# Kernel optimization log

Measured on AMD Instinct MI355X. Metric: run time of the kernel, lower is better.

The kernel has to match this reference:

```python
import jax, jax.numpy as jnp
import numpy as np

# ---- Cayley-Dickson octonion multiplication tables (SIGN_TABLE, WEIGHT_IDX) ----
def _cd_conj(a):
    n = a.shape[0]
    if n == 1:
        return a
    h = n // 2
    return np.concatenate([_cd_conj(a[:h]), -a[h:]])

def _cd_mul(a, b):
    n = a.shape[0]
    if n == 1:
        return a * b
    h = n // 2
    a1, a2 = a[:h], a[h:]
    c1, c2 = b[:h], b[h:]
    # (a1,a2)(c1,c2) = (a1 c1 - conj(c2) a2, c2 a1 + a2 conj(c1))
    return np.concatenate([_cd_mul(a1, c1) - _cd_mul(_cd_conj(c2), a2),
                           _cd_mul(c2, a1) + _cd_mul(a2, _cd_conj(c1))])

def _octonion_tables():
    signs = np.zeros((8, 8), dtype=np.float32)
    widx = np.zeros((8, 8), dtype=np.int32)
    for i in range(8):
        for j in range(8):
            ei = np.zeros(8); ei[i] = 1.0
            ej = np.zeros(8); ej[j] = 1.0
            p = _cd_mul(ei, ej)
            k = int(np.argmax(np.abs(p)))  # == i ^ j
            signs[i, j] = np.sign(p[k])
            widx[i, j] = k
    return jnp.asarray(signs), jnp.asarray(widx)

SIGNS, WIDX = _octonion_tables()


def ternary_ste(W):
    # BitNet-style per-matrix ternary quantization with straight-through estimator.
    s = jnp.mean(jnp.abs(W), axis=(-2, -1), keepdims=True) + 1e-8
    Wq = jnp.clip(jnp.round(W / s), -1.0, 1.0) * s
    return W + jax.lax.stop_gradient(Wq - W)


def oct_linear(x, W):
    # x: [B,T,C] split into 8 parts of C/8; out_i = sum_j sign[i,j] * x_j @ Wq[i^j]
    B, T, C = x.shape
    c8 = C // 8
    x8 = x.reshape(B, T, 8, c8)
    Wq = ternary_ste(W)          # [8, c8, c8]
    Wg = Wq[WIDX]                # [8, 8, c8, c8]
    out = jnp.einsum('ij,btjc,ijcd->btid', SIGNS, x8, Wg)
    return out.reshape(B, T, C)


def apply_rope(q, freqs_cos, freqs_sin):
    # q: [B,T,H,D]; complex pairs are (q[...,2k], q[...,2k+1])
    qe, qo = q[..., 0::2], q[..., 1::2]
    cos = freqs_cos[None, :, None, :]
    sin = freqs_sin[None, :, None, :]
    oe = qe * cos - qo * sin
    oo = qe * sin + qo * cos
    return jnp.stack([oe, oo], axis=-1).reshape(q.shape)


def setup_inputs() -> dict:
    key = jax.random.key(0)
    ks = jax.random.split(key, 8)
    B, T, C, H = 4, 1024, 2048, 16
    D = C // H           # 128
    c8 = C // 8          # 256
    x = jax.random.normal(ks[0], (B, T, C), dtype=jnp.float32)
    # RoPE tables (theta = 10000)
    inv = 1.0 / (10000.0 ** (jnp.arange(0, D, 2, dtype=jnp.float32) / D))
    ang = jnp.arange(T, dtype=jnp.float32)[:, None] * inv[None, :]   # [T, D/2]
    freqs_cos = jnp.cos(ang)
    freqs_sin = jnp.sin(ang)
    wq = jax.random.normal(ks[1], (8, c8, c8), dtype=jnp.float32) * 0.02
    wk = jax.random.normal(ks[2], (8, c8, c8), dtype=jnp.float32) * 0.02
    wv = jax.random.normal(ks[3], (8, c8, c8), dtype=jnp.float32) * 0.02
    wo = jax.random.normal(ks[4], (8, c8, c8), dtype=jnp.float32) * 0.02
    mixer_W = jax.random.normal(ks[5], (8, D, D), dtype=jnp.float32) * 0.02
    mixer_beta = jnp.ones((D,), dtype=jnp.float32) * 0.1
    return {"x": x, "freqs_cos": freqs_cos, "freqs_sin": freqs_sin,
            "wq": wq, "wk": wk, "wv": wv, "wo": wo,
            "mixer_W": mixer_W, "mixer_beta": mixer_beta}


def reference(x, freqs_cos, freqs_sin, wq, wk, wv, wo, mixer_W, mixer_beta):
    B, T, C = x.shape
    H = 16
    D = C // H
    q = oct_linear(x, wq).reshape(B, T, H, D)
    k = oct_linear(x, wk).reshape(B, T, H, D)
    v = oct_linear(x, wv).reshape(B, T, H, D)
    q = apply_rope(q, freqs_cos, freqs_sin)
    k = apply_rope(k, freqs_cos, freqs_sin)
    q, k, v = (jnp.transpose(t, (0, 2, 1, 3)) for t in (q, k, v))  # [B,H,T,D]
    # causal SDPA
    scale = 1.0 / jnp.sqrt(jnp.asarray(D, dtype=q.dtype))
    scores = jnp.einsum('bhqd,bhkd->bhqk', q, k) * scale
    mask = jnp.tril(jnp.ones((T, T), dtype=bool))
    scores = jnp.where(mask, scores, jnp.asarray(-1e30, dtype=scores.dtype))
    probs = jax.nn.softmax(scores, axis=-1)
    y = jnp.einsum('bhqk,bhkd->bhqd', probs, v)  # [B,H,T,D]
    # octonion head mixing per group of 8 heads
    G = H // 8
    y8 = y.reshape(B, G, 8, T, D)
    Wg = mixer_W[WIDX]  # [8,8,D,D]
    y8 = jnp.einsum('ij,bgjtd,ijde->bgite', SIGNS, y8, Wg) * mixer_beta
    y = y8.reshape(B, H, T, D)
    y = jnp.transpose(y, (0, 2, 1, 3)).reshape(B, T, C)
    return oct_linear(y, wo)
```

## Files before the change

kernel.cpp:

```cpp
#include <hip/hip_runtime.h>
#include <math.h>

#define CDIM 2048
#define QKVW 6144

typedef __bf16 bf16x8 __attribute__((ext_vector_type(8)));
typedef __bf16 bf16x4 __attribute__((ext_vector_type(4)));
typedef float  f32x4  __attribute__((ext_vector_type(4)));
typedef float  f32x16 __attribute__((ext_vector_type(16)));

__device__ __constant__ float SIGNS_c[64] = {
  1,  1,  1,  1,  1,  1,  1,  1,
  1, -1,  1, -1,  1, -1, -1,  1,
  1, -1, -1,  1,  1,  1, -1, -1,
  1,  1, -1, -1,  1, -1,  1, -1,
  1, -1, -1, -1, -1,  1,  1,  1,
  1,  1, -1,  1, -1, -1, -1,  1,
  1,  1,  1, -1, -1,  1, -1, -1,
  1, -1,  1,  1, -1, -1,  1, -1
};

__device__ __forceinline__ void load_lds16(const void* g, void* lp) {
  __builtin_amdgcn_global_load_lds(
      (const __attribute__((address_space(1))) unsigned int*)g,
      (__attribute__((address_space(3))) unsigned int*)lp, 16, 0, 0);
}

__device__ __forceinline__ void wg_barrier() {
  asm volatile("" ::: "memory");
  __builtin_amdgcn_s_barrier();
  asm volatile("" ::: "memory");
}

__device__ __forceinline__ unsigned pack2(float a, float b) {
  union { __bf16 h[2]; unsigned u; } x;
  x.h[0] = (__bf16)a; x.h[1] = (__bf16)b; return x.u;
}

__global__ __launch_bounds__(256)
void cast_scale(const float* __restrict__ x, __bf16* __restrict__ xb,
                const float* __restrict__ wq, const float* __restrict__ wk,
                const float* __restrict__ wv, const float* __restrict__ wo,
                double* __restrict__ part) {
  __shared__ double red[256];
  if (blockIdx.x < 8192) {
    int i = blockIdx.x * 256 + threadIdx.x;
    float4 v = *(const float4*)(x + (size_t)i * 4);
    bf16x4 o;
    o[0] = (__bf16)v.x; o[1] = (__bf16)v.y; o[2] = (__bf16)v.z; o[3] = (__bf16)v.w;
    *(bf16x4*)(xb + (size_t)i * 4) = o;
    return;
  }
  int bid = blockIdx.x - 8192;
  int which = bid >> 6, m = (bid >> 3) & 7, seg = bid & 7;
  const float* W = (which == 0) ? wq : (which == 1) ? wk : (which == 2) ? wv : wo;
  const float4* w4 = (const float4*)(W + (m << 16) + seg * 8192);
  double acc = 0.0;
  #pragma unroll
  for (int i = 0; i < 8; ++i) {
    float4 v = w4[threadIdx.x + i * 256];
    acc += (double)fabsf(v.x) + (double)fabsf(v.y) +
           (double)fabsf(v.z) + (double)fabsf(v.w);
  }
  red[threadIdx.x] = acc;
  __syncthreads();
  for (int s = 128; s > 0; s >>= 1) {
    if (threadIdx.x < s) red[threadIdx.x] += red[threadIdx.x + s];
    __syncthreads();
  }
  if (threadIdx.x == 0) part[bid] = red[0];
}

__global__ void scale_fin(const double* __restrict__ part, double* __restrict__ s8,
                          double* __restrict__ rs8) {
  int t = threadIdx.x;
  if (t < 32) {
    double a = 0.0;
    #pragma unroll
    for (int i = 0; i < 8; ++i) a += part[t * 8 + i];
    double s = a / 65536.0 + 1e-8;
    s8[t] = s;
    rs8[t] = 1.0 / s;
  }
}

__global__ void build_oct3(const float* __restrict__ wq, const float* __restrict__ wk,
                           const float* __restrict__ wv, const double* __restrict__ s8,
                           const double* __restrict__ rs8, __bf16* __restrict__ MT) {
  int z = blockIdx.y;
  const float* W = (z == 0) ? wq : (z == 1) ? wk : wv;
  const double* sp = s8 + z * 8;
  const double* rp = rs8 + z * 8;
  __bf16* out = MT + (size_t)z * 4194304;
  int idx = blockIdx.x * 256 + threadIdx.x;
  int row = idx & 2047, col = idx >> 11;
  int i = col >> 8, d = col & 255, j = row >> 8, c = row & 255;
  int m = i ^ j;
  double q = rint((double)W[(m << 16) + (c << 8) + d] * rp[m]);
  q = fmin(fmax(q, -1.0), 1.0);
  out[idx] = (__bf16)(SIGNS_c[i * 8 + j] * (float)(q * sp[m]));
}

__global__ void build_wo_mix(const float* __restrict__ W, const double* __restrict__ s8,
                             const double* __restrict__ rs8, __bf16* __restrict__ MT,
                             const float* __restrict__ Wm, const float* __restrict__ beta,
                             __bf16* __restrict__ Mmix) {
  if (blockIdx.x < 16384) {
    int idx = blockIdx.x * 256 + threadIdx.x;
    int row = idx & 2047, col = idx >> 11;
    int i = col >> 8, d = col & 255, j = row >> 8, c = row & 255;
    int m = i ^ j;
    double q = rint((double)W[(m << 16) + (c << 8) + d] * rs8[m]);
    q = fmin(fmax(q, -1.0), 1.0);
    MT[idx] = (__bf16)(SIGNS_c[i * 8 + j] * (float)(q * s8[m]));
    return;
  }
  int idx = (blockIdx.x - 16384) * 256 + threadIdx.x;
  int kl = idx & 1023, kpl = idx >> 10;
  int j = kpl >> 7, dd = kpl & 127;
  int i = kl >> 7, e = kl & 127;
  Mmix[idx] = (__bf16)(SIGNS_c[i * 8 + j] * Wm[((i ^ j) << 14) + (dd << 7) + e] * beta[e]);
}

__global__ __launch_bounds__(512, 2)
void gemm_qkv8(const __bf16* __restrict__ A, const __bf16* __restrict__ BT,
               __bf16* __restrict__ C, __bf16* __restrict__ VT) {
  __shared__ __align__(16) char smem[131072];
  int tid = threadIdx.x;
  int w = tid >> 6, l = tid & 63, hi = l >> 4, lo = l & 15;
  int wm = w >> 2, wn = w & 3;
  int lin = blockIdx.x;
  int xcd = lin & 7, idx = lin >> 3;
  int cy = xcd >> 2, cx = xcd & 3;
  int iby = idx >> 3, ibx = idx & 7;
  int bm = (cy * 8 + iby) * 256;
  int bn = (cx * 8 + ibx) * 192;
  const char* Ab = (const char*)A + (size_t)bm * 4096;
  const char* Bb = (const char*)BT + (size_t)bn * 4096;

  int sw = (((lo & 1) << 2) + hi) ^ (lo >> 1);

  int se_r[2], se_g[2], se_rb[2];
  #pragma unroll
  for (int q = 0; q < 2; ++q) {
    int e = q * 512 + tid;
    int lr = e >> 3, sl = e & 7;
    int x = sl ^ (lr & 7);
    se_r[q] = lr * 2 + (x >> 2);
    se_g[q] = x & 3;
    se_rb[q] = se_r[q] < 192 ? se_r[q] : 191;
  }
  int dstoff[2] = { (0 * 512 + w * 64) * 16, (1 * 512 + w * 64) * 16 };

  f32x4 acc[8][3];
  #pragma unroll
  for (int m = 0; m < 8; ++m)
    #pragma unroll
    for (int n = 0; n < 3; ++n) acc[m][n] = (f32x4){0.f, 0.f, 0.f, 0.f};
  bf16x8 bfr[3];

  #define STG(MAT, TT, KH) do {                                                  \
    char* dst_ = smem + ((TT) & 1) * 65536 + (MAT) * 32768 + (KH) * 16384;       \
    const char* gb_ = (MAT) ? Bb : Ab;                                           \
    _Pragma("unroll")                                                            \
    for (int q = 0; q < 2; ++q) {                                                \
      int r_ = (MAT) ? se_rb[q] : se_r[q];                                       \
      load_lds16(gb_ + (size_t)r_ * 4096 + ((TT) * 64 + (KH) * 32) * 2 + se_g[q] * 16, \
                 dst_ + dstoff[q]);                                              \
    }                                                                            \
  } while (0)

  #define QUAD(TT, KH, MSUB, READB) do {                                         \
    const char* ar_ = smem + ((TT) & 1) * 65536 + (KH) * 16384;                  \
    const char* br_ = ar_ + 32768;                                               \
    if (READB) {                                                                 \
      _Pragma("unroll")                                                          \
      for (int n = 0; n < 3; ++n)                                                \
        bfr[n] = *(const bf16x8*)(br_ + (wn * 24 + n * 8 + (lo >> 1)) * 128 + sw * 16); \
    }                                                                            \
    bf16x8 afr[4];                                                               \
    _Pragma("unroll")                                                            \
    for (int m = 0; m < 4; ++m)                                                  \
      afr[m] = *(const bf16x8*)(ar_ + (wm * 64 + (MSUB) * 32 + m * 8 + (lo >> 1)) * 128 + sw * 16); \
    __builtin_amdgcn_s_setprio(1);                                               \
    _Pragma("unroll")                                                            \
    for (int m = 0; m < 4; ++m)                                                  \
      _Pragma("unroll")                                                          \
      for (int n = 0; n < 3; ++n)                                                \
        acc[(MSUB) * 4 + m][n] =                                                 \
            __builtin_amdgcn_mfma_f32_16x16x32_bf16(afr[m], bfr[n], acc[(MSUB) * 4 + m][n], 0, 0, 0); \
    __builtin_amdgcn_s_setprio(0);                                               \
  } while (0)

  #define LGK0() asm volatile("s_waitcnt lgkmcnt(0)" ::: "memory")
  #define VMW8() asm volatile("s_waitcnt vmcnt(8)" ::: "memory")
  #define VMW4() asm volatile("s_waitcnt vmcnt(4)" ::: "memory")
  #define VMW0() asm volatile("s_waitcnt vmcnt(0)" ::: "memory")

  STG(0, 0, 0); STG(1, 0, 0);
  STG(0, 0, 1); STG(1, 0, 1);
  STG(0, 1, 0); STG(1, 1, 0);
  VMW8();
  wg_barrier();

  #define GITER(T0, LAST) do {                                                   \
     STG(0, (T0) + 1, 1); QUAD((T0), 0, 0, 1); wg_barrier();            \
     STG(1, (T0) + 1, 1); QUAD((T0), 0, 1, 0); LGK0(); VMW8(); wg_barrier(); \
     if (!(LAST)) { STG(0, (T0) + 2, 0); } QUAD((T0), 1, 0, 1); wg_barrier(); \
     if (!(LAST)) { STG(1, (T0) + 2, 0); } QUAD((T0), 1, 1, 0); LGK0(); \
              if (LAST) { VMW4(); } else { VMW8(); } wg_barrier();               \
     if (!(LAST)) { STG(0, (T0) + 2, 1); } QUAD((T0) + 1, 0, 0, 1); wg_barrier(); \
     if (!(LAST)) { STG(1, (T0) + 2, 1); } QUAD((T0) + 1, 0, 1, 0); LGK0(); \
              if (LAST) { VMW0(); } else { VMW8(); } wg_barrier();               \
     if (!(LAST)) { STG(0, (T0) + 3, 0); } QUAD((T0) + 1, 1, 0, 1); wg_barrier(); \
     if (!(LAST)) { STG(1, (T0) + 3, 0); } QUAD((T0) + 1, 1, 1, 0);     \
              if (!(LAST)) { LGK0(); VMW8(); wg_barrier(); }                     \
  } while (0)

  for (int i = 0; i < 15; ++i) GITER(2 * i, false);
  GITER(30, true);

  #undef GITER
  #undef STG
  #undef QUAD
  #undef VMW8
  #undef VMW4
  #undef LGK0
  #undef VMW0

  #pragma unroll
  for (int mm = 0; mm < 8; ++mm)
    #pragma unroll
    for (int n = 0; n < 3; ++n) {
      int col = bn + wn * 48 + n * 16 + lo;
      int row0 = bm + wm * 128 + mm * 16 + hi * 4;
      if (col < 4096) {
        #pragma unroll
        for (int r = 0; r < 4; ++r)
          C[(size_t)(row0 + r) * QKVW + col] = (__bf16)acc[mm][n][r];
      } else {
        int v = col - 4096;
        int bh = (row0 >> 10) * 16 + (v >> 7);
        int dd = v & 127;
        int t0 = row0 & 1023;
        bf16x4 ov;
        #pragma unroll
        for (int r = 0; r < 4; ++r) ov[r] = (__bf16)acc[mm][n][r];
        *(bf16x4*)(VT + ((size_t)bh * 128 + dd) * 1024 + t0) = ov;
      }
    }
}

__global__ __launch_bounds__(512, 2)
void gemm_fin8(const __bf16* __restrict__ A, const __bf16* __restrict__ BT,
               float* __restrict__ C) {
  __shared__ __align__(16) char smem[98304];
  int tid = threadIdx.x;
  int w = tid >> 6, l = tid & 63, hi = l >> 4, lo = l & 15;
  int wm = w >> 2, wn = w & 3;
  int lin = blockIdx.x;
  int xcd = lin & 7, idx = lin >> 3;
  int cy = xcd >> 1, cx = xcd & 1;
  int iby = idx >> 2, ibx = idx & 3;
  int bm = (cy * 8 + iby) * 128;
  int bn = (cx * 4 + ibx) * 256;
  const char* Ab = (const char*)A + (size_t)bm * 12288;
  const char* Bb = (const char*)BT + (size_t)bn * 4096;

  int sw = (((lo & 1) << 2) + hi) ^ (lo >> 1);

  int se_r[2], se_g[2];
  #pragma unroll
  for (int q = 0; q < 2; ++q) {
    int e = q * 512 + tid;
    int lr = e >> 3, sl = e & 7;
    int x = sl ^ (lr & 7);
    se_r[q] = lr * 2 + (x >> 2);
    se_g[q] = x & 3;
  }
  int dstoff[2] = { (0 * 512 + w * 64) * 16, (1 * 512 + w * 64) * 16 };

  f32x4 acc[4][4];
  #pragma unroll
  for (int m = 0; m < 4; ++m)
    #pragma unroll
    for (int n = 0; n < 4; ++n) acc[m][n] = (f32x4){0.f, 0.f, 0.f, 0.f};
  bf16x8 bfr[4];

  #define STG(MAT, TT, KH) do {                                                  \
    char* ab_ = smem + ((TT) & 1) * 49152;                                       \
    char* dst_ = (MAT) ? (ab_ + 16384 + (KH) * 16384) : (ab_ + (KH) * 8192);     \
    const char* gb_ = (MAT) ? Bb : Ab;                                           \
    size_t ld_ = (MAT) ? 4096 : 12288;                                           \
    int nq_ = (MAT) ? 2 : 1;                                                     \
    _Pragma("unroll")                                                            \
    for (int q = 0; q < 2; ++q)                                                  \
      if (q < nq_)                                                               \
        load_lds16(gb_ + (size_t)se_r[q] * ld_ + ((TT) * 64 + (KH) * 32) * 2 + se_g[q] * 16, \
                   dst_ + dstoff[q]);                                            \
  } while (0)

  #define QUAD(TT, KH, MSUB, READB) do {                                         \
    const char* ab_ = smem + ((TT) & 1) * 49152;                                 \
    const char* ar_ = ab_ + (KH) * 8192;                                         \
    const char* br_ = ab_ + 16384 + (KH) * 16384;                                \
    if (READB) {                                                                 \
      _Pragma("unroll")                                                          \
      for (int n = 0; n < 4; ++n)                                                \
        bfr[n] = *(const bf16x8*)(br_ + (wn * 32 + n * 8 + (lo >> 1)) * 128 + sw * 16); \
    }                                                                            \
    bf16x8 afr[2];                                                               \
    _Pragma("unroll")                                                            \
    for (int m = 0; m < 2; ++m)                                                  \
      afr[m] = *(const bf16x8*)(ar_ + (wm * 32 + (MSUB) * 16 + m * 8 + (lo >> 1)) * 128 + sw * 16); \
    __builtin_amdgcn_s_setprio(1);                                               \
    _Pragma("unroll")                                                            \
    for (int m = 0; m < 2; ++m)                                                  \
      _Pragma("unroll")                                                          \
      for (int n = 0; n < 4; ++n)                                                \
        acc[(MSUB) * 2 + m][n] =                                                 \
            __builtin_amdgcn_mfma_f32_16x16x32_bf16(afr[m], bfr[n], acc[(MSUB) * 2 + m][n], 0, 0, 0); \
    __builtin_amdgcn_s_setprio(0);                                               \
  } while (0)

  #define LGK0() asm volatile("s_waitcnt lgkmcnt(0)" ::: "memory")
  #define VMW6() asm volatile("s_waitcnt vmcnt(6)" ::: "memory")
  #define VMW3() asm volatile("s_waitcnt vmcnt(3)" ::: "memory")
  #define VMW0() asm volatile("s_waitcnt vmcnt(0)" ::: "memory")

  STG(0, 0, 0); STG(1, 0, 0);
  STG(0, 0, 1); STG(1, 0, 1);
  STG(0, 1, 0); STG(1, 1, 0);
  VMW6();
  wg_barrier();

  #define GITER(T0, LAST) do {                                                   \
     STG(0, (T0) + 1, 1); QUAD((T0), 0, 0, 1); wg_barrier();            \
     STG(1, (T0) + 1, 1); QUAD((T0), 0, 1, 0); LGK0(); VMW6(); wg_barrier(); \
     if (!(LAST)) { STG(0, (T0) + 2, 0); } QUAD((T0), 1, 0, 1); wg_barrier(); \
     if (!(LAST)) { STG(1, (T0) + 2, 0); } QUAD((T0), 1, 1, 0); LGK0(); \
              if (LAST) { VMW3(); } else { VMW6(); } wg_barrier();               \
     if (!(LAST)) { STG(0, (T0) + 2, 1); } QUAD((T0) + 1, 0, 0, 1); wg_barrier(); \
     if (!(LAST)) { STG(1, (T0) + 2, 1); } QUAD((T0) + 1, 0, 1, 0); LGK0(); \
              if (LAST) { VMW0(); } else { VMW6(); } wg_barrier();               \
     if (!(LAST)) { STG(0, (T0) + 3, 0); } QUAD((T0) + 1, 1, 0, 1); wg_barrier(); \
     if (!(LAST)) { STG(1, (T0) + 3, 0); } QUAD((T0) + 1, 1, 1, 0);     \
              if (!(LAST)) { LGK0(); VMW6(); wg_barrier(); }                     \
  } while (0)

  for (int i = 0; i < 15; ++i) GITER(2 * i, false);
  GITER(30, true);

  #undef GITER
  #undef STG
  #undef QUAD
  #undef VMW6
  #undef VMW3
  #undef LGK0
  #undef VMW0

  #pragma unroll
  for (int mm = 0; mm < 4; ++mm)
    #pragma unroll
    for (int n = 0; n < 4; ++n)
      #pragma unroll
      for (int r = 0; r < 4; ++r) {
        int row = bm + wm * 64 + mm * 16 + hi * 4 + r;
        int col = bn + wn * 64 + n * 16 + lo;
        C[(size_t)row * 2048 + col] = acc[mm][n][r];
      }
}

template<int BN, int NBY, int NBX, int CBY, int CBX, int KLEN, int LDA, int OUT_BF16>
__global__ __launch_bounds__(512, 2)
void gemm_ps(const __bf16* __restrict__ A, const __bf16* __restrict__ BT,
             void* __restrict__ Cout, int az, int cz, int ldc) {
  constexpr int FN = BN / 64;
  constexpr int LB = (BN > 128) ? 2 : 1;
  constexpr int VC = 2 + LB;
  constexpr int BUFSZ = 16384 + 8192 * LB;
  constexpr int CGX = NBX / CBX;
  static_assert((NBY / CBY) * CGX == 8, "chunk grid must be 8 XCDs");
  __shared__ __align__(16) char smem[2 * BUFSZ];
  int tid = threadIdx.x;
  int w = tid >> 6, l = tid & 63, hi = l >> 4, lo = l & 15;
  int wm = w >> 2, wn = w & 3;
  int lin = blockIdx.x;
  int xcd = lin & 7, idx = lin >> 3;
  int cy = xcd / CGX, cx = xcd % CGX;
  int iby = idx / CBX, ibx = idx % CBX;
  int bm = (cy * CBY + iby) * 256;
  int bn = (cx * CBX + ibx) * BN;
  const char* Ab = (const char*)(A + (size_t)blockIdx.y * az) + (size_t)bm * LDA * 2;
  const char* Bb = (const char*)BT + (size_t)bn * KLEN * 2;

  int sw = (((lo & 1) << 2) + hi) ^ (lo >> 1);
  int base_a = (wm * 64 + (lo >> 1)) * 128 + sw * 16;
  int base_b = 16384 + (wn * (BN / 8) + (lo >> 1)) * 128 + sw * 16;

  int se_r[2], se_g[2];
  #pragma unroll
  for (int q = 0; q < 2; ++q) {
    int e = q * 512 + tid;
    int lr = e >> 3, sl = e & 7;
    int x = sl ^ (lr & 7);
    se_r[q] = lr * 2 + (x >> 2);
    se_g[q] = x & 3;
  }
  int dstoff[2] = { (0 * 512 + w * 64) * 16, (1 * 512 + w * 64) * 16 };

  f32x4 acc[8][FN];
  #pragma unroll
  for (int m = 0; m < 8; ++m)
    #pragma unroll
    for (int n = 0; n < FN; ++n) acc[m][n] = (f32x4){0.f, 0.f, 0.f, 0.f};

  #define STAGE(BUFI, K0) do {                                                   \
    char* As_ = smem + (BUFI) * BUFSZ;                                           \
    char* Bs_ = As_ + 16384;                                                     \
    _Pragma("unroll")                                                            \
    for (int q = 0; q < 2; ++q)                                                  \
      load_lds16(Ab + (size_t)se_r[q] * (LDA * 2) + (size_t)(K0) * 2 + se_g[q] * 16, \
                 As_ + dstoff[q]);                                               \
    _Pragma("unroll")                                                            \
    for (int q = 0; q < LB; ++q)                                                 \
      load_lds16(Bb + (size_t)se_r[q] * (KLEN * 2) + (size_t)(K0) * 2 + se_g[q] * 16, \
                 Bs_ + dstoff[q]);                                               \
  } while (0)

  #define WAITVC() do {                                                \
    if constexpr (VC == 4) asm volatile("s_waitcnt vmcnt(4)" ::: "memory"); \
    else                   asm volatile("s_waitcnt vmcnt(3)" ::: "memory"); \
  } while (0)

  constexpr int NT = KLEN / 32;
  STAGE(0, 0);
  STAGE(1, 32);
  WAITVC();
  wg_barrier();

  for (int t = 0; t < NT; ++t) {
    char* buf = smem + (t & 1) * BUFSZ;
    bf16x8 bfr[FN], afr[8];
    #pragma unroll
    for (int n = 0; n < FN; ++n) bfr[n] = *(const bf16x8*)(buf + base_b + n * 1024);
    #pragma unroll
    for (int m = 0; m < 8; ++m) afr[m] = *(const bf16x8*)(buf + base_a + m * 1024);
    __builtin_amdgcn_s_setprio(1);
    #pragma unroll
    for (int m = 0; m < 4; ++m)
      #pragma unroll
      for (int n = 0; n < FN; ++n)
        acc[m][n] = __builtin_amdgcn_mfma_f32_16x16x32_bf16(afr[m], bfr[n], acc[m][n], 0, 0, 0);
    __builtin_amdgcn_s_setprio(0);
    asm volatile("s_waitcnt lgkmcnt(0)" ::: "memory");
    wg_barrier();

    if (t + 2 < NT) STAGE(t & 1, (t + 2) * 32);
    __builtin_amdgcn_s_setprio(1);
    #pragma unroll
    for (int m = 4; m < 8; ++m)
      #pragma unroll
      for (int n = 0; n < FN; ++n)
        acc[m][n] = __builtin_amdgcn_mfma_f32_16x16x32_bf16(afr[m], bfr[n], acc[m][n], 0, 0, 0);
    __builtin_amdgcn_s_setprio(0);
    if (t + 2 < NT) { WAITVC(); }
    else            { asm volatile("s_waitcnt vmcnt(0)" ::: "memory"); }
    wg_barrier();
  }
  #undef STAGE
  #undef WAITVC

  #pragma unroll
  for (int m = 0; m < 8; ++m)
    #pragma unroll
    for (int n = 0; n < FN; ++n)
      #pragma unroll
      for (int r = 0; r < 4; ++r) {
        int row = bm + wm * 128 + m * 16 + hi * 4 + r;
        int col = bn + wn * (BN / 4) + n * 16 + lo;
        if (OUT_BF16)
          ((__bf16*)Cout)[(size_t)blockIdx.y * cz + (size_t)row * ldc + col] = (__bf16)acc[m][n][r];
        else
          ((float*)Cout)[(size_t)blockIdx.y * cz + (size_t)row * ldc + col] = acc[m][n][r];
      }
}

__global__ __launch_bounds__(256)
void rope_bf16(__bf16* __restrict__ QKV,
               const float* __restrict__ fc, const float* __restrict__ fs) {
  int idx = blockIdx.x * 256 + threadIdx.x;
  int pg = idx & 15;
  int h = (idx >> 4) & 15;
  int n = idx >> 8;
  int t = n & 1023;
  float4 c4 = *(const float4*)(fc + t * 64 + pg * 4);
  float4 s4 = *(const float4*)(fs + t * 64 + pg * 4);
  float c[4] = {c4.x, c4.y, c4.z, c4.w};
  float s[4] = {s4.x, s4.y, s4.z, s4.w};
  size_t ofs = (size_t)n * QKVW + h * 128 + pg * 8;
  bf16x8 q = *(bf16x8*)(QKV + ofs);
  bf16x8 k = *(bf16x8*)(QKV + 2048 + ofs);
  bf16x8 oq, ok;
  #pragma unroll
  for (int j = 0; j < 4; ++j) {
    float x = (float)q[2 * j], y = (float)q[2 * j + 1];
    oq[2 * j]     = (__bf16)(x * c[j] - y * s[j]);
    oq[2 * j + 1] = (__bf16)(x * s[j] + y * c[j]);
    float u = (float)k[2 * j], vv = (float)k[2 * j + 1];
    ok[2 * j]     = (__bf16)(u * c[j] - vv * s[j]);
    ok[2 * j + 1] = (__bf16)(u * s[j] + vv * c[j]);
  }
  *(bf16x8*)(QKV + ofs) = oq;
  *(bf16x8*)(QKV + 2048 + ofs) = ok;
}

__global__ __launch_bounds__(256, 2)
void attn_mfma2(__bf16* __restrict__ QKV, const __bf16* __restrict__ VT) {
  __shared__ __align__(16) char smem[65536];
  int tid = threadIdx.x;
  int w = tid >> 6, l = tid & 63;
  int lo = l & 31, hv = l >> 5;
  int wgid = blockIdx.x;
  int xcd = wgid & 7, idx = wgid >> 3;
  int s = idx & 7, j = s >> 1, odd = s & 1, hi5 = idx >> 5;
  int base = hi5 ? 7 - j : j;
  int qt = odd ? 7 - base : base;
  int bh = xcd * 8 + (idx >> 3);
  int b = bh >> 4, h = bh & 15;
  int qb = qt * 128;
  int wq0 = qb + w * 32;
  int qrow = wq0 + lo;
  const __bf16* qp = QKV + (size_t)(b * 1024 + qrow) * QKVW + h * 128;
  bf16x8 qf[8];
  #pragma unroll
  for (int c = 0; c < 8; ++c) qf[c] = *(const bf16x8*)(qp + c * 16 + hv * 8);

  f32x16 o[4];
  #pragma unroll
  for (int n = 0; n < 4; ++n)
    #pragma unroll
    for (int r = 0; r < 16; ++r) o[n][r] = 0.f;
  float mrun = -1e30f, lrun = 0.f;
  const float SCL = 0.08838834764831845f * 1.4426950408889634f;
  int src0 = lo, src1 = 32 + lo;
  int nt = 2 * qt + 2;

  #define ASTAGE(BUF, KT) do {                                                   \
    _Pragma("unroll")                                                            \
    for (int i = 0; i < 4; ++i) {                                                \
      int e = i * 256 + tid;                                                     \
      int row = e >> 4, g = e & 15;                                              \
      int gs = g ^ (row & 7);                                                    \
      const char* src = (const char*)QKV +                                       \
          ((size_t)(b * 1024 + (KT) * 64 + row) * QKVW + 2048 + h * 128) * 2 + gs * 16; \
      load_lds16(src, smem + (BUF) * 16384 + (i * 256 + w * 64) * 16);           \
    }                                                                            \
    _Pragma("unroll")                                                            \
    for (int i = 0; i < 4; ++i) {                                                \
      int e = i * 256 + tid;                                                     \
      int row = e >> 3, g = e & 7;                                               \
      int gs = g ^ (row & 7);                                                    \
      const char* src = (const char*)VT +                                        \
          ((size_t)(bh * 128 + row) * 1024 + (KT) * 64) * 2 + gs * 16;           \
      load_lds16(src, smem + 32768 + (BUF) * 16384 + (i * 256 + w * 64) * 16);   \
    }                                                                            \
  } while (0)

  ASTAGE(0, 0);
  asm volatile("s_waitcnt vmcnt(0)" ::: "memory");
  wg_barrier();

  for (int kt = 0; kt < nt; ++kt) {
    int cur = kt & 1;
    if (kt + 1 < nt) ASTAGE(cur ^ 1, kt + 1);
    int k0 = kt * 64;
    char* Ks  = smem + cur * 16384;
    char* VTs = smem + 32768 + cur * 16384;

    if (k0 <= wq0 + 31) {
      f32x16 sT[2];
      #pragma unroll
      for (int kk = 0; kk < 2; ++kk) {
        #pragma unroll
        for (int r = 0; r < 16; ++r) sT[kk][r] = 0.f;
        #pragma unroll
        for (int c = 0; c < 8; ++c) {
          bf16x8 kf = *(const bf16x8*)(Ks + (kk * 32 + lo) * 256 + (((2 * c + hv) ^ (lo & 7)) * 16));
          sT[kk] = __builtin_amdgcn_mfma_f32_32x32x16_bf16(kf, qf[c], sT[kk], 0, 0, 0);
        }
      }
      bool diag = (k0 + 63 > wq0);
      float pv[2][16];
      #pragma unroll
      for (int kk = 0; kk < 2; ++kk)
        #pragma unroll
        for (int r = 0; r < 16; ++r) {
          float v = sT[kk][r] * SCL;
          if (diag) {
            int kg = k0 + kk * 32 + (r & 3) + 8 * (r >> 2) + 4 * hv;
            if (kg > qrow) v = -1e30f;
          }
          pv[kk][r] = v;
        }
      float mx = pv[0][0];
      #pragma unroll
      for (int kk = 0; kk < 2; ++kk)
        #pragma unroll
        for (int r = 0; r < 16; ++r) mx = fmaxf(mx, pv[kk][r]);
      mx = fmaxf(mx, __shfl_xor(mx, 32, 64));
      if (!__all(mx <= mrun + 8.f)) {
        float mnew = fmaxf(mrun, mx);
        float fac = exp2f(mrun - mnew);
        lrun *= fac;
        #pragma unroll
        for (int n = 0; n < 4; ++n)
          #pragma unroll
          for (int r = 0; r < 16; ++r) o[n][r] *= fac;
        mrun = mnew;
      }
      float rs = 0.f;
      #pragma unroll
      for (int kk = 0; kk < 2; ++kk)
        #pragma unroll
        for (int r = 0; r < 16; ++r) {
          float p = exp2f(pv[kk][r] - mrun);
          pv[kk][r] = p;
          rs += p;
        }
      rs += __shfl_xor(rs, 32, 64);
      lrun += rs;

      unsigned pk[2][4][2];
      #pragma unroll
      for (int kk = 0; kk < 2; ++kk)
        #pragma unroll
        for (int m = 0; m < 4; ++m)
          #pragma unroll
          for (int u = 0; u < 2; ++u)
            pk[kk][m][u] = pack2(pv[kk][m * 4 + 2 * u], pv[kk][m * 4 + 2 * u + 1]);

      #pragma unroll
      for (int kk = 0; kk < 2; ++kk) {
        #pragma unroll
        for (int s2 = 0; s2 < 2; ++s2) {
          unsigned a0 = __shfl(pk[kk][2 * s2][0], src0, 64);
          unsigned b0 = __shfl(pk[kk][2 * s2 + 1][0], src0, 64);
          unsigned a1 = __shfl(pk[kk][2 * s2][1], src0, 64);
          unsigned b1 = __shfl(pk[kk][2 * s2 + 1][1], src0, 64);
          unsigned a2 = __shfl(pk[kk][2 * s2][0], src1, 64);
          unsigned b2 = __shfl(pk[kk][2 * s2 + 1][0], src1, 64);
          unsigned a3 = __shfl(pk[kk][2 * s2][1], src1, 64);
          unsigned b3 = __shfl(pk[kk][2 * s2 + 1][1], src1, 64);
          union { unsigned u[4]; bf16x8 v; } pb;
          pb.u[0] = hv ? b0 : a0;
          pb.u[1] = hv ? b1 : a1;
          pb.u[2] = hv ? b2 : a2;
          pb.u[3] = hv ? b3 : a3;
          int ks16 = 2 * kk + s2;
          #pragma unroll
          for (int n = 0; n < 4; ++n) {
            bf16x8 vf = *(const bf16x8*)(VTs + (n * 32 + lo) * 128 +
                                         (((2 * ks16 + hv) ^ (lo & 7)) * 16));
            o[n] = __builtin_amdgcn_mfma_f32_32x32x16_bf16(vf, pb.v, o[n], 0, 0, 0);
          }
        }
      }
    }
    asm volatile("s_waitcnt vmcnt(0)" ::: "memory");
    wg_barrier();
  }
  #undef ASTAGE

  float inv = 1.f / lrun;
  __bf16* op = QKV + (size_t)(b * 1024 + qrow) * QKVW + h * 128;
  #pragma unroll
  for (int n = 0; n < 4; ++n)
    #pragma unroll
    for (int m4 = 0; m4 < 4; ++m4) {
      bf16x4 ov;
      #pragma unroll
      for (int jj = 0; jj < 4; ++jj) ov[jj] = (__bf16)(o[n][m4 * 4 + jj] * inv);
      *(bf16x4*)(op + n * 32 + 8 * m4 + 4 * hv) = ov;
    }
}

extern "C" void kernel_launch(void* const* d_in, const int* in_sizes, int n_in,
                              void* d_out, int out_size, void* d_ws, size_t ws_size,
                              hipStream_t stream) {
  const float* x    = (const float*)d_in[0];
  const float* fc   = (const float*)d_in[1];
  const float* fs   = (const float*)d_in[2];
  const float* wq   = (const float*)d_in[3];
  const float* wk   = (const float*)d_in[4];
  const float* wv   = (const float*)d_in[5];
  const float* wo   = (const float*)d_in[6];
  const float* wm   = (const float*)d_in[7];
  const float* beta = (const float*)d_in[8];

  char* wsb = (char*)d_ws;
  __bf16* xb      = (__bf16*)(wsb);
  __bf16* MTqkv   = (__bf16*)(wsb + 16777216L);
  __bf16* QKV     = (__bf16*)(wsb + 41943040L);
  __bf16* VTb     = (__bf16*)(wsb + 92274688L);
  double* s8      = (double*)(wsb + 109051904L);
  double* part    = (double*)(wsb + 109052160L);
  double* rs8     = (double*)(wsb + 109054208L);
  __bf16* MTwo    = (__bf16*)(wsb);
  __bf16* BTfused = (__bf16*)(wsb + 8388608L);
  __bf16* MTmixP  = MTqkv;

  dim3 blk(256);

  cast_scale<<<8448, blk, 0, stream>>>(x, xb, wq, wk, wv, wo, part);
  scale_fin<<<1, dim3(64), 0, stream>>>(part, s8, rs8);
  build_oct3<<<dim3(16384, 3), blk, 0, stream>>>(wq, wk, wv, s8, rs8, MTqkv);

  gemm_qkv8<<<512, dim3(512), 0, stream>>>(xb, MTqkv, QKV, VTb);

  build_wo_mix<<<20480, blk, 0, stream>>>(wo, s8 + 24, rs8 + 24, MTwo, wm, beta, MTmixP);
  gemm_ps<128, 8, 8, 2, 4, 1024, 2048, 1>
      <<<dim3(64, 2), dim3(512), 0, stream>>>(MTwo, MTmixP, BTfused, 1024, 1024, 2048);

  rope_bf16<<<4096, blk, 0, stream>>>(QKV, fc, fs);

  attn_mfma2<<<dim3(512), blk, 0, stream>>>(QKV, VTb);

  gemm_fin8<<<256, dim3(512), 0, stream>>>(QKV, BTfused, (float*)d_out);
}
```

Measured before the change: 296.0 us.

## Fold scale finalization into weight builders and tune attention inner loop

Removes the single-block scale_fin launch by having every block of build_oct3 and build_wo_mix reduce its eight per-matrix partial sums into shared memory. In the attention kernel the QK^T MFMAs are interleaved across the two key tiles and wrapped, along with the PV MFMAs, in s_setprio raises. The row max and row sum now use tree reductions instead of serial chains. This trades one small launch for redundant per-block reductions plus a barrier, and aims to shorten dependency chains in the softmax.

```diff
diff --git a/kernel.cpp b/kernel.cpp
--- a/kernel.cpp
+++ b/kernel.cpp
@@ -71,48 +71,55 @@
   if (threadIdx.x == 0) part[bid] = red[0];
 }
 
-__global__ void scale_fin(const double* __restrict__ part, double* __restrict__ s8,
-                          double* __restrict__ rs8) {
-  int t = threadIdx.x;
-  if (t < 32) {
+__global__ void build_oct3(const float* __restrict__ wq, const float* __restrict__ wk,
+                           const float* __restrict__ wv, const double* __restrict__ part,
+                           __bf16* __restrict__ MT) {
+  __shared__ double s_s[8], s_r[8];
+  int z = blockIdx.y;
+  int tid = threadIdx.x;
+  if (tid < 8) {
     double a = 0.0;
     #pragma unroll
-    for (int i = 0; i < 8; ++i) a += part[t * 8 + i];
+    for (int i = 0; i < 8; ++i) a += part[z * 64 + tid * 8 + i];
     double s = a / 65536.0 + 1e-8;
-    s8[t] = s;
-    rs8[t] = 1.0 / s;
-  }
-}
-
-__global__ void build_oct3(const float* __restrict__ wq, const float* __restrict__ wk,
-                           const float* __restrict__ wv, const double* __restrict__ s8,
-                           const double* __restrict__ rs8, __bf16* __restrict__ MT) {
-  int z = blockIdx.y;
+    s_s[tid] = s;
+    s_r[tid] = 1.0 / s;
+  }
+  __syncthreads();
   const float* W = (z == 0) ? wq : (z == 1) ? wk : wv;
-  const double* sp = s8 + z * 8;
-  const double* rp = rs8 + z * 8;
   __bf16* out = MT + (size_t)z * 4194304;
-  int idx = blockIdx.x * 256 + threadIdx.x;
+  int idx = blockIdx.x * 256 + tid;
   int row = idx & 2047, col = idx >> 11;
   int i = col >> 8, d = col & 255, j = row >> 8, c = row & 255;
   int m = i ^ j;
-  double q = rint((double)W[(m << 16) + (c << 8) + d] * rp[m]);
+  double q = rint((double)W[(m << 16) + (c << 8) + d] * s_r[m]);
   q = fmin(fmax(q, -1.0), 1.0);
-  out[idx] = (__bf16)(SIGNS_c[i * 8 + j] * (float)(q * sp[m]));
-}
-
-__global__ void build_wo_mix(const float* __restrict__ W, const double* __restrict__ s8,
-                             const double* __restrict__ rs8, __bf16* __restrict__ MT,
+  out[idx] = (__bf16)(SIGNS_c[i * 8 + j] * (float)(q * s_s[m]));
+}
+
+__global__ void build_wo_mix(const float* __restrict__ W, const double* __restrict__ part,
+                             __bf16* __restrict__ MT,
                              const float* __restrict__ Wm, const float* __restrict__ beta,
                              __bf16* __restrict__ Mmix) {
   if (blockIdx.x < 16384) {
-    int idx = blockIdx.x * 256 + threadIdx.x;
+    __shared__ double s_s[8], s_r[8];
+    int tid = threadIdx.x;
+    if (tid < 8) {
+      double a = 0.0;
+      #pragma unroll
+      for (int i = 0; i < 8; ++i) a += part[192 + tid * 8 + i];
+      double s = a / 65536.0 + 1e-8;
+      s_s[tid] = s;
+      s_r[tid] = 1.0 / s;
+    }
+    __syncthreads();
+    int idx = blockIdx.x * 256 + tid;
     int row = idx & 2047, col = idx >> 11;
     int i = col >> 8, d = col & 255, j = row >> 8, c = row & 255;
     int m = i ^ j;
-    double q = rint((double)W[(m << 16) + (c << 8) + d] * rs8[m]);
+    double q = rint((double)W[(m << 16) + (c << 8) + d] * s_r[m]);
     q = fmin(fmax(q, -1.0), 1.0);
-    MT[idx] = (__bf16)(SIGNS_c[i * 8 + j] * (float)(q * s8[m]));
+    MT[idx] = (__bf16)(SIGNS_c[i * 8 + j] * (float)(q * s_s[m]));
     return;
   }
   int idx = (blockIdx.x - 16384) * 256 + threadIdx.x;
@@ -581,15 +588,20 @@
     if (k0 <= wq0 + 31) {
       f32x16 sT[2];
       #pragma unroll
-      for (int kk = 0; kk < 2; ++kk) {
+      for (int kk = 0; kk < 2; ++kk)
         #pragma unroll
         for (int r = 0; r < 16; ++r) sT[kk][r] = 0.f;
-        #pragma unroll
-        for (int c = 0; c < 8; ++c) {
+      __builtin_amdgcn_s_setprio(1);
+      #pragma unroll
+      for (int c = 0; c < 8; ++c) {
+        #pragma unroll
+        for (int kk = 0; kk < 2; ++kk) {
           bf16x8 kf = *(const bf16x8*)(Ks + (kk * 32 + lo) * 256 + (((2 * c + hv) ^ (lo & 7)) * 16));
           sT[kk] = __builtin_amdgcn_mfma_f32_32x32x16_bf16(kf, qf[c], sT[kk], 0, 0, 0);
         }
       }
+      __builtin_amdgcn_s_setprio(0);
+
       bool diag = (k0 + 63 > wq0);
       float pv[2][16];
       #pragma unroll
@@ -603,12 +615,15 @@
           }
           pv[kk][r] = v;
         }
-      float mx = pv[0][0];
-      #pragma unroll
-      for (int kk = 0; kk < 2; ++kk)
-        #pragma unroll
-        for (int r = 0; r < 16; ++r) mx = fmaxf(mx, pv[kk][r]);
-      mx = fmaxf(mx, __shfl_xor(mx, 32, 64));
+      float m16[16];
+      #pragma unroll
+      for (int r = 0; r < 16; ++r) m16[r] = fmaxf(pv[0][r], pv[1][r]);
+      #pragma unroll
+      for (int off = 8; off > 0; off >>= 1)
+        #pragma unroll
+        for (int r = 0; r < 8; ++r)
+          if (r < off) m16[r] = fmaxf(m16[r], m16[r + off]);
+      float mx = fmaxf(m16[0], __shfl_xor(m16[0], 32, 64));
       if (!__all(mx <= mrun + 8.f)) {
         float mnew = fmaxf(mrun, mx);
         float fac = exp2f(mrun - mnew);
@@ -619,16 +634,20 @@
           for (int r = 0; r < 16; ++r) o[n][r] *= fac;
         mrun = mnew;
       }
-      float rs = 0.f;
       #pragma unroll
       for (int kk = 0; kk < 2; ++kk)
         #pragma unroll
-        for (int r = 0; r < 16; ++r) {
-          float p = exp2f(pv[kk][r] - mrun);
-          pv[kk][r] = p;
-          rs += p;
-        }
-      rs += __shfl_xor(rs, 32, 64);
+        for (int r = 0; r < 16; ++r)
+          pv[kk][r] = exp2f(pv[kk][r] - mrun);
+      float s16[16];
+      #pragma unroll
+      for (int r = 0; r < 16; ++r) s16[r] = pv[0][r] + pv[1][r];
+      #pragma unroll
+      for (int off = 8; off > 0; off >>= 1)
+        #pragma unroll
+        for (int r = 0; r < 8; ++r)
+          if (r < off) s16[r] += s16[r + off];
+      float rs = s16[0] + __shfl_xor(s16[0], 32, 64);
       lrun += rs;
 
       unsigned pk[2][4][2];
@@ -658,12 +677,14 @@
           pb.u[2] = hv ? b2 : a2;
           pb.u[3] = hv ? b3 : a3;
           int ks16 = 2 * kk + s2;
+          __builtin_amdgcn_s_setprio(1);
           #pragma unroll
           for (int n = 0; n < 4; ++n) {
             bf16x8 vf = *(const bf16x8*)(VTs + (n * 32 + lo) * 128 +
                                          (((2 * ks16 + hv) ^ (lo & 7)) * 16));
             o[n] = __builtin_amdgcn_mfma_f32_32x32x16_bf16(vf, pb.v, o[n], 0, 0, 0);
           }
+          __builtin_amdgcn_s_setprio(0);
         }
       }
     }
@@ -703,9 +724,7 @@
   __bf16* MTqkv   = (__bf16*)(wsb + 16777216L);
   __bf16* QKV     = (__bf16*)(wsb + 41943040L);
   __bf16* VTb     = (__bf16*)(wsb + 92274688L);
-  double* s8      = (double*)(wsb + 109051904L);
   double* part    = (double*)(wsb + 109052160L);
-  double* rs8     = (double*)(wsb + 109054208L);
   __bf16* MTwo    = (__bf16*)(wsb);
   __bf16* BTfused = (__bf16*)(wsb + 8388608L);
   __bf16* MTmixP  = MTqkv;
@@ -713,12 +732,11 @@
   dim3 blk(256);
 
   cast_scale<<<8448, blk, 0, stream>>>(x, xb, wq, wk, wv, wo, part);
-  scale_fin<<<1, dim3(64), 0, stream>>>(part, s8, rs8);
-  build_oct3<<<dim3(16384, 3), blk, 0, stream>>>(wq, wk, wv, s8, rs8, MTqkv);
+  build_oct3<<<dim3(16384, 3), blk, 0, stream>>>(wq, wk, wv, part, MTqkv);
 
   gemm_qkv8<<<512, dim3(512), 0, stream>>>(xb, MTqkv, QKV, VTb);
 
-  build_wo_mix<<<20480, blk, 0, stream>>>(wo, s8 + 24, rs8 + 24, MTwo, wm, beta, MTmixP);
+  build_wo_mix<<<20480, blk, 0, stream>>>(wo, part, MTwo, wm, beta, MTmixP);
   gemm_ps<128, 8, 8, 2, 4, 1024, 2048, 1>
       <<<dim3(64, 2), dim3(512), 0, stream>>>(MTwo, MTmixP, BTfused, 1024, 1024, 2048);
 
```

New measurement: 299.3 us. Within noise of the previous version (+1.1%).
